# Kernel optimization log

Hardware: AMD Instinct MI355X
Metric: run time of the kernel (lower is better)

## Reference

```python
import jax, jax.numpy as jnp
from jax import lax
import numpy as np

FILTER_SIZE = 3
PAD = FILTER_SIZE // 2


def _smooth(off, filt):
    # ReflectionPad2d(pad) -> conv2d(padding=pad) -> crop pad:-pad  == same-size smoothing
    x = jnp.pad(off, ((0, 0), (0, 0), (PAD, PAD), (PAD, PAD)), mode='reflect')
    y = lax.conv_general_dilated(x, filt, window_strides=(1, 1),
                                 padding=[(PAD, PAD), (PAD, PAD)],
                                 dimension_numbers=('NCHW', 'OIHW', 'NCHW'))
    return y[:, :, PAD:-PAD, PAD:-PAD]


def _grid_sample(img, gx, gy):
    # img: [C,H,W]; gx,gy: [N,H,W] normalized to [-1,1].
    # Bilinear, align_corners=True, zero padding (torch 1.x default at repo time).
    C, H, W = img.shape
    ix = (gx + 1.0) * 0.5 * (W - 1)
    iy = (gy + 1.0) * 0.5 * (H - 1)
    x0 = jnp.floor(ix); y0 = jnp.floor(iy)
    x1 = x0 + 1.0;      y1 = y0 + 1.0
    wx1 = ix - x0; wx0 = 1.0 - wx1
    wy1 = iy - y0; wy0 = 1.0 - wy1

    def gather(xi, yi):
        valid = ((xi >= 0) & (xi <= W - 1) & (yi >= 0) & (yi <= H - 1)).astype(img.dtype)
        xc = jnp.clip(xi, 0, W - 1).astype(jnp.int32)
        yc = jnp.clip(yi, 0, H - 1).astype(jnp.int32)
        return img[:, yc, xc] * valid[None]  # [C,N,H,W]

    out = (gather(x0, y0) * (wx0 * wy0)[None] +
           gather(x1, y0) * (wx1 * wy0)[None] +
           gather(x0, y1) * (wx0 * wy1)[None] +
           gather(x1, y1) * (wx1 * wy1)[None])
    return out  # [C,N,H,W]


def setup_inputs() -> dict:
    key = jax.random.key(0)
    k1, k2, k3 = jax.random.split(key, 3)
    C, H, W = 16, 512, 960
    F2 = FILTER_SIZE * FILTER_SIZE
    right_input = jax.random.normal(k1, (1, C, H, W), jnp.float32)
    offset_x = jax.random.uniform(k2, (1, 1, H, W), jnp.float32) * 64.0  # disparity-like
    offset_y = jax.random.uniform(k3, (1, 1, H, W), jnp.float32) * 8.0
    x_coordinate = jnp.tile(jnp.arange(W, dtype=jnp.float32)[None, None, None, :], (1, 1, H, 1))
    y_coordinate = jnp.tile(jnp.arange(H, dtype=jnp.float32)[None, None, :, None], (1, 1, 1, W))
    # one-hot neighbour extraction filters: channel i picks neighbour i of the 3x3 patch
    neighbour_extraction_filter = jnp.eye(F2, dtype=jnp.float32).reshape(F2, 1, FILTER_SIZE, FILTER_SIZE)
    return {'right_input': right_input, 'offset_x': offset_x, 'offset_y': offset_y,
            'x_coordinate': x_coordinate, 'y_coordinate': y_coordinate,
            'neighbour_extraction_filter': neighbour_extraction_filter}


def reference(right_input, offset_x, offset_y, x_coordinate, y_coordinate, neighbour_extraction_filter):
    H, W = offset_x.shape[2], offset_x.shape[3]
    sx = _smooth(offset_x, neighbour_extraction_filter)  # [1,F2,H,W]
    sy = _smooth(offset_y, neighbour_extraction_filter)  # [1,F2,H,W]
    coord_x = jnp.clip(x_coordinate - sx, 0.0, W - 1)
    coord_y = jnp.clip(y_coordinate - sy, 0.0, H - 1)
    half_w = W / 2.0; half_h = H / 2.0
    gx = (coord_x - half_w) / half_w  # [1,F2,H,W]
    gy = (coord_y - half_h) / half_h
    # grid batch = 1*F2; instead of repeating right_input F2 times, gather from the
    # single image for all F2 grids at once, then patch-vote (mean over F2).
    rec = _grid_sample(right_input[0], gx[0], gy[0])  # [C,F2,H,W]
    return jnp.mean(rec, axis=1)[None]  # [1,C,H,W]
```

## Files before the change

kernel.cpp:

```cpp
#include <hip/hip_runtime.h>
#include <hip/hip_fp16.h>

#define CH 16
#define HH 512
#define WW 960
#define HW (HH * WW)

#define TR 8
#define TC 64
#define RROWS 18
#define RCOLS 136
#define NHALF (RROWS * RCOLS * 2)

typedef __fp16 v2hf __attribute__((ext_vector_type(2)));
typedef _Float16 h2r __attribute__((ext_vector_type(2)));

__device__ __forceinline__ unsigned pkrtz_u(float a, float b) {
  v2hf r = __builtin_amdgcn_cvt_pkrtz(a, b);
  return __builtin_bit_cast(unsigned, r);
}
__device__ __forceinline__ __half2 u2h(unsigned u) {
  return __builtin_bit_cast(__half2, u);
}

__global__ __launch_bounds__(512, 4) void recon_fused_f16(
    const float* __restrict__ img,
    const float* __restrict__ offx,
    const float* __restrict__ offy,
    float* __restrict__ out) {
  __shared__ uint4 lds[NHALF];

  const int hwid = blockIdx.x + blockIdx.y * 15;
  const int tile = (hwid & 7) * 120 + (hwid >> 3);
  const int tx = tile % 15, ty = tile / 15;
  const int x0b = tx * TC, y0b = ty * TR;
  const int tid = threadIdx.x;
  const int ylo = y0b - 9, xlo = x0b - 68;

  for (int it = 0; it < 10; ++it) {
    const int f = it * 512 + tid;
    if (f < NHALF) {
      const int half = f & 1;
      const int p    = f >> 1;
      const int row  = p / RCOLS;
      const int col  = p - row * RCOLS;
      const int gr = min(max(ylo + row, 0), HH - 1);
      const int gc = min(max(xlo + col, 0), WW - 1);
      const float* src = img + (half * 8) * HW + gr * WW + gc;
      uint4 o;
      o.x = pkrtz_u(src[0 * HW], src[1 * HW]);
      o.y = pkrtz_u(src[2 * HW], src[3 * HW]);
      o.z = pkrtz_u(src[4 * HW], src[5 * HW]);
      o.w = pkrtz_u(src[6 * HW], src[7 * HW]);
      lds[f] = o;
    }
  }
  __syncthreads();

  const int pixl = tid & 63;
  const int rowl = tid >> 6;
  const int x = x0b + pixl;
  const int y = y0b + rowl;
  const int cA = tid & 1;

  const float fxs = (float)(WW - 1) / (float)WW;
  const float fys = (float)(HH - 1) / (float)HH;

  float accA[8], accB[8];
#pragma unroll
  for (int i = 0; i < 8; ++i) { accA[i] = 0.f; accB[i] = 0.f; }

#pragma unroll
  for (int di = -1; di <= 1; ++di) {
    int rr = y + di;
    rr = (rr < 0) ? 1 : ((rr >= HH) ? (HH - 2) : rr);
    __half2 hA[4], hB[4];
#pragma unroll
    for (int i = 0; i < 4; ++i) { hA[i] = u2h(0u); hB[i] = u2h(0u); }

#pragma unroll
    for (int dj = -1; dj <= 1; ++dj) {
      int cc = x + dj;
      cc = (cc < 0) ? 1 : ((cc >= WW) ? (WW - 2) : cc);
      const int o = rr * WW + cc;
      const float sx = offx[o];
      const float sy = offy[o];
      const float cx = fminf(fmaxf((float)x - sx, 0.0f), (float)(WW - 1));
      const float cy = fminf(fmaxf((float)y - sy, 0.0f), (float)(HH - 1));
      const float ix = cx * fxs;
      const float iy = cy * fys;
      const float fx0 = floorf(ix);
      const float fy0 = floorf(iy);
      const float wx1 = ix - fx0, wx0 = 1.0f - wx1;
      const float wy1 = iy - fy0, wy0 = 1.0f - wy1;
      const int u00 = ((int)fy0 - ylo) * RCOLS + ((int)fx0 - xlo);

      const __half2 w00 = u2h(pkrtz_u(wx0 * wy0, wx0 * wy0));
      const __half2 w10 = u2h(pkrtz_u(wx1 * wy0, wx1 * wy0));
      const __half2 w01 = u2h(pkrtz_u(wx0 * wy1, wx0 * wy1));
      const __half2 w11 = u2h(pkrtz_u(wx1 * wy1, wx1 * wy1));

#define CORNER(UIDX, Wh)                                     \
  {                                                          \
    const uint4 qa = lds[((UIDX) << 1) + cA];                \
    const uint4 qb = lds[((UIDX) << 1) + (cA ^ 1)];          \
    hA[0] = __hfma2(u2h(qa.x), (Wh), hA[0]);                 \
    hA[1] = __hfma2(u2h(qa.y), (Wh), hA[1]);                 \
    hA[2] = __hfma2(u2h(qa.z), (Wh), hA[2]);                 \
    hA[3] = __hfma2(u2h(qa.w), (Wh), hA[3]);                 \
    hB[0] = __hfma2(u2h(qb.x), (Wh), hB[0]);                 \
    hB[1] = __hfma2(u2h(qb.y), (Wh), hB[1]);                 \
    hB[2] = __hfma2(u2h(qb.z), (Wh), hB[2]);                 \
    hB[3] = __hfma2(u2h(qb.w), (Wh), hB[3]);                 \
  }
      CORNER(u00, w00)
      CORNER(u00 + 1, w10)
      CORNER(u00 + RCOLS, w01)
      CORNER(u00 + RCOLS + 1, w11)
#undef CORNER
    }
#pragma unroll
    for (int i = 0; i < 4; ++i) {
      const h2r a = __builtin_bit_cast(h2r, hA[i]);
      const h2r b = __builtin_bit_cast(h2r, hB[i]);
      accA[2 * i]     += (float)a.x;
      accA[2 * i + 1] += (float)a.y;
      accB[2 * i]     += (float)b.x;
      accB[2 * i + 1] += (float)b.y;
    }
  }

  const float s = 1.0f / 9.0f;
  const int po = y * WW + x;
#pragma unroll
  for (int j = 0; j < 8; ++j) {
    const float lo = (cA ? accB[j] : accA[j]) * s;
    const float hi = (cA ? accA[j] : accB[j]) * s;
    out[j * HW + po]       = lo;
    out[(j + 8) * HW + po] = hi;
  }
}

extern "C" void kernel_launch(void* const* d_in, const int* in_sizes, int n_in,
                              void* d_out, int out_size, void* d_ws, size_t ws_size,
                              hipStream_t stream) {
  const float* right = (const float*)d_in[0];
  const float* offx  = (const float*)d_in[1];
  const float* offy  = (const float*)d_in[2];
  float* out = (float*)d_out;

  const dim3 grid(WW / TC, HH / TR);
  recon_fused_f16<<<grid, 512, 0, stream>>>(right, offx, offy, out);
}
```

Measured before the change: 117.6 us.

## Process channels in two 8-channel chunks to halve LDS footprint and raise occupancy

The shared tile now holds only 8 fp16 channels per pixel instead of 16, and the kernel loops twice: it stages one channel half into shared memory, samples and writes 8 output channels, then restages the other half. Shared memory per block drops from about 78KB to about 39KB and the launch bound asks for 8 blocks per CU instead of 4, aiming for more resident waves to hide gather latency. In exchange the offset loads and the bilinear weight arithmetic are done twice, and an extra barrier serialises the two staging phases.

```diff
diff --git a/kernel.cpp b/kernel.cpp
--- a/kernel.cpp
+++ b/kernel.cpp
@@ -10,7 +10,7 @@
 #define TC 64
 #define RROWS 18
 #define RCOLS 136
-#define NHALF (RROWS * RCOLS * 2)
+#define NSLOT (RROWS * RCOLS)
 
 typedef __fp16 v2hf __attribute__((ext_vector_type(2)));
 typedef _Float16 h2r __attribute__((ext_vector_type(2)));
@@ -23,12 +23,12 @@
   return __builtin_bit_cast(__half2, u);
 }
 
-__global__ __launch_bounds__(512, 4) void recon_fused_f16(
+__global__ __launch_bounds__(512, 8) void recon_fused_f16(
     const float* __restrict__ img,
     const float* __restrict__ offx,
     const float* __restrict__ offy,
     float* __restrict__ out) {
-  __shared__ uint4 lds[NHALF];
+  __shared__ uint4 lds[NSLOT];
 
   const int hwid = blockIdx.x + blockIdx.y * 15;
   const int tile = (hwid & 7) * 120 + (hwid >> 3);
@@ -37,107 +37,97 @@
   const int tid = threadIdx.x;
   const int ylo = y0b - 9, xlo = x0b - 68;
 
-  for (int it = 0; it < 10; ++it) {
-    const int f = it * 512 + tid;
-    if (f < NHALF) {
-      const int half = f & 1;
-      const int p    = f >> 1;
-      const int row  = p / RCOLS;
-      const int col  = p - row * RCOLS;
-      const int gr = min(max(ylo + row, 0), HH - 1);
-      const int gc = min(max(xlo + col, 0), WW - 1);
-      const float* src = img + (half * 8) * HW + gr * WW + gc;
-      uint4 o;
-      o.x = pkrtz_u(src[0 * HW], src[1 * HW]);
-      o.y = pkrtz_u(src[2 * HW], src[3 * HW]);
-      o.z = pkrtz_u(src[4 * HW], src[5 * HW]);
-      o.w = pkrtz_u(src[6 * HW], src[7 * HW]);
-      lds[f] = o;
-    }
-  }
-  __syncthreads();
-
   const int pixl = tid & 63;
   const int rowl = tid >> 6;
   const int x = x0b + pixl;
   const int y = y0b + rowl;
-  const int cA = tid & 1;
+  const int po = y * WW + x;
 
   const float fxs = (float)(WW - 1) / (float)WW;
   const float fys = (float)(HH - 1) / (float)HH;
-
-  float accA[8], accB[8];
-#pragma unroll
-  for (int i = 0; i < 8; ++i) { accA[i] = 0.f; accB[i] = 0.f; }
+  const float s = 1.0f / 9.0f;
 
 #pragma unroll
-  for (int di = -1; di <= 1; ++di) {
-    int rr = y + di;
-    rr = (rr < 0) ? 1 : ((rr >= HH) ? (HH - 2) : rr);
-    __half2 hA[4], hB[4];
+  for (int chunk = 0; chunk < 2; ++chunk) {
 #pragma unroll
-    for (int i = 0; i < 4; ++i) { hA[i] = u2h(0u); hB[i] = u2h(0u); }
+    for (int it = 0; it < 5; ++it) {
+      const int f = it * 512 + tid;
+      if (f < NSLOT) {
+        const int row = f / RCOLS;
+        const int col = f - row * RCOLS;
+        const int gr = min(max(ylo + row, 0), HH - 1);
+        const int gc = min(max(xlo + col, 0), WW - 1);
+        const float* src = img + (chunk * 8) * HW + gr * WW + gc;
+        uint4 o;
+        o.x = pkrtz_u(src[0 * HW], src[1 * HW]);
+        o.y = pkrtz_u(src[2 * HW], src[3 * HW]);
+        o.z = pkrtz_u(src[4 * HW], src[5 * HW]);
+        o.w = pkrtz_u(src[6 * HW], src[7 * HW]);
+        lds[f] = o;
+      }
+    }
+    __syncthreads();
+
+    float acc[8];
+#pragma unroll
+    for (int i = 0; i < 8; ++i) acc[i] = 0.f;
 
 #pragma unroll
-    for (int dj = -1; dj <= 1; ++dj) {
-      int cc = x + dj;
-      cc = (cc < 0) ? 1 : ((cc >= WW) ? (WW - 2) : cc);
-      const int o = rr * WW + cc;
-      const float sx = offx[o];
-      const float sy = offy[o];
-      const float cx = fminf(fmaxf((float)x - sx, 0.0f), (float)(WW - 1));
-      const float cy = fminf(fmaxf((float)y - sy, 0.0f), (float)(HH - 1));
-      const float ix = cx * fxs;
-      const float iy = cy * fys;
-      const float fx0 = floorf(ix);
-      const float fy0 = floorf(iy);
-      const float wx1 = ix - fx0, wx0 = 1.0f - wx1;
-      const float wy1 = iy - fy0, wy0 = 1.0f - wy1;
-      const int u00 = ((int)fy0 - ylo) * RCOLS + ((int)fx0 - xlo);
+    for (int di = -1; di <= 1; ++di) {
+      int rr = y + di;
+      rr = (rr < 0) ? 1 : ((rr >= HH) ? (HH - 2) : rr);
+      __half2 h[4];
+#pragma unroll
+      for (int i = 0; i < 4; ++i) h[i] = u2h(0u);
 
-      const __half2 w00 = u2h(pkrtz_u(wx0 * wy0, wx0 * wy0));
-      const __half2 w10 = u2h(pkrtz_u(wx1 * wy0, wx1 * wy0));
-      const __half2 w01 = u2h(pkrtz_u(wx0 * wy1, wx0 * wy1));
-      const __half2 w11 = u2h(pkrtz_u(wx1 * wy1, wx1 * wy1));
+#pragma unroll
+      for (int dj = -1; dj <= 1; ++dj) {
+        int cc = x + dj;
+        cc = (cc < 0) ? 1 : ((cc >= WW) ? (WW - 2) : cc);
+        const int o = rr * WW + cc;
+        const float sx = offx[o];
+        const float sy = offy[o];
+        const float cx = fminf(fmaxf((float)x - sx, 0.0f), (float)(WW - 1));
+        const float cy = fminf(fmaxf((float)y - sy, 0.0f), (float)(HH - 1));
+        const float ix = cx * fxs;
+        const float iy = cy * fys;
+        const float fx0 = floorf(ix);
+        const float fy0 = floorf(iy);
+        const float wx1 = ix - fx0, wx0 = 1.0f - wx1;
+        const float wy1 = iy - fy0, wy0 = 1.0f - wy1;
+        const int u00 = ((int)fy0 - ylo) * RCOLS + ((int)fx0 - xlo);
 
-#define CORNER(UIDX, Wh)                                     \
-  {                                                          \
-    const uint4 qa = lds[((UIDX) << 1) + cA];                \
-    const uint4 qb = lds[((UIDX) << 1) + (cA ^ 1)];          \
-    hA[0] = __hfma2(u2h(qa.x), (Wh), hA[0]);                 \
-    hA[1] = __hfma2(u2h(qa.y), (Wh), hA[1]);                 \
-    hA[2] = __hfma2(u2h(qa.z), (Wh), hA[2]);                 \
-    hA[3] = __hfma2(u2h(qa.w), (Wh), hA[3]);                 \
-    hB[0] = __hfma2(u2h(qb.x), (Wh), hB[0]);                 \
-    hB[1] = __hfma2(u2h(qb.y), (Wh), hB[1]);                 \
-    hB[2] = __hfma2(u2h(qb.z), (Wh), hB[2]);                 \
-    hB[3] = __hfma2(u2h(qb.w), (Wh), hB[3]);                 \
+        const __half2 w00 = u2h(pkrtz_u(wx0 * wy0, wx0 * wy0));
+        const __half2 w10 = u2h(pkrtz_u(wx1 * wy0, wx1 * wy0));
+        const __half2 w01 = u2h(pkrtz_u(wx0 * wy1, wx0 * wy1));
+        const __half2 w11 = u2h(pkrtz_u(wx1 * wy1, wx1 * wy1));
+
+#define CORNER(UIDX, Wh)                          \
+  {                                               \
+    const uint4 q = lds[(UIDX)];                  \
+    h[0] = __hfma2(u2h(q.x), (Wh), h[0]);         \
+    h[1] = __hfma2(u2h(q.y), (Wh), h[1]);         \
+    h[2] = __hfma2(u2h(q.z), (Wh), h[2]);         \
+    h[3] = __hfma2(u2h(q.w), (Wh), h[3]);         \
   }
-      CORNER(u00, w00)
-      CORNER(u00 + 1, w10)
-      CORNER(u00 + RCOLS, w01)
-      CORNER(u00 + RCOLS + 1, w11)
+        CORNER(u00, w00)
+        CORNER(u00 + 1, w10)
+        CORNER(u00 + RCOLS, w01)
+        CORNER(u00 + RCOLS + 1, w11)
 #undef CORNER
+      }
+#pragma unroll
+      for (int i = 0; i < 4; ++i) {
+        const h2r a = __builtin_bit_cast(h2r, h[i]);
+        acc[2 * i]     += (float)a.x;
+        acc[2 * i + 1] += (float)a.y;
+      }
     }
+
 #pragma unroll
-    for (int i = 0; i < 4; ++i) {
-      const h2r a = __builtin_bit_cast(h2r, hA[i]);
-      const h2r b = __builtin_bit_cast(h2r, hB[i]);
-      accA[2 * i]     += (float)a.x;
-      accA[2 * i + 1] += (float)a.y;
-      accB[2 * i]     += (float)b.x;
-      accB[2 * i + 1] += (float)b.y;
-    }
-  }
+    for (int j = 0; j < 8; ++j) out[(chunk * 8 + j) * HW + po] = acc[j] * s;
 
-  const float s = 1.0f / 9.0f;
-  const int po = y * WW + x;
-#pragma unroll
-  for (int j = 0; j < 8; ++j) {
-    const float lo = (cA ? accB[j] : accA[j]) * s;
-    const float hi = (cA ? accA[j] : accB[j]) * s;
-    out[j * HW + po]       = lo;
-    out[(j + 8) * HW + po] = hi;
+    if (chunk == 0) __syncthreads();
   }
 }
 
```

New measurement: 120.5 us. +2.4%, slower.
